# Kernel optimization log

Measured on AMD Instinct MI355X. Metric: run time of the kernel, lower is better.

## Reference

```python
import jax, jax.numpy as jnp
import numpy as np

N_NODES = 50000
N_EDGES = 800000
N_GRAPHS = 512
D = 128
NUM_GIN_LAYERS = 4
BN_EPS = 1e-5


def setup_inputs() -> dict:
    key = jax.random.key(0)
    ks = jax.random.split(key, 10)
    h = jax.random.normal(ks[0], (N_NODES, D), dtype=jnp.float32)
    src = jax.random.randint(ks[1], (N_EDGES,), 0, N_NODES, dtype=jnp.int32)
    dst = jax.random.randint(ks[2], (N_EDGES,), 0, N_NODES, dtype=jnp.int32)
    graph_id = jnp.sort(jax.random.randint(ks[3], (N_NODES,), 0, N_GRAPHS, dtype=jnp.int32))
    scale = 1.0 / np.sqrt(D)
    W1s = jax.random.normal(ks[4], (NUM_GIN_LAYERS, D, D), dtype=jnp.float32) * scale
    W2s = jax.random.normal(ks[5], (NUM_GIN_LAYERS, D, D), dtype=jnp.float32) * scale
    bn1_g = jnp.ones((NUM_GIN_LAYERS, D), jnp.float32)
    bn1_b = jnp.zeros((NUM_GIN_LAYERS, D), jnp.float32)
    bn2_g = jnp.ones((NUM_GIN_LAYERS, D), jnp.float32)
    bn2_b = jnp.zeros((NUM_GIN_LAYERS, D), jnp.float32)
    pred_W = jax.random.normal(ks[6], (NUM_GIN_LAYERS + 1, D, D), dtype=jnp.float32) * scale
    pred_b = jnp.zeros((NUM_GIN_LAYERS + 1, D), jnp.float32)
    return {"h": h, "src": src, "dst": dst, "graph_id": graph_id,
            "W1s": W1s, "W2s": W2s, "bn1_g": bn1_g, "bn1_b": bn1_b,
            "bn2_g": bn2_g, "bn2_b": bn2_b, "pred_W": pred_W, "pred_b": pred_b}


def _batch_norm(x, gamma, beta):
    # training-mode BN over the node axis
    mean = jnp.mean(x, axis=0)
    var = jnp.var(x, axis=0)
    return (x - mean) * jax.lax.rsqrt(var + BN_EPS) * gamma + beta


def reference(h, src, dst, graph_id, W1s, W2s, bn1_g, bn1_b, bn2_g, bn2_b, pred_W, pred_b):
    n = h.shape[0]
    hidden_rep = [h]
    for i in range(NUM_GIN_LAYERS):
        # GINConv, eps=0: (1+eps)*h + sum over in-neighbors (scatter-sum over edges)
        agg = jax.ops.segment_sum(h[src], dst, num_segments=n)
        z = h + agg
        # two-layer MLP: Linear(no bias) -> BN -> ReLU -> Linear(no bias)
        z = jax.nn.relu(_batch_norm(z @ W1s[i], bn1_g[i], bn1_b[i]))
        z = z @ W2s[i]
        # outer BN + ReLU
        h = jax.nn.relu(_batch_norm(z, bn2_g[i], bn2_b[i]))
        hidden_rep.append(h)
    # graph readout: per-graph max pool over each layer's representation,
    # then per-layer linear prediction summed (dropout is identity in eval)
    score = jnp.zeros((N_GRAPHS, pred_W.shape[-1]), h.dtype)
    for i, hr in enumerate(hidden_rep):
        pooled = jax.ops.segment_max(hr, graph_id, num_segments=N_GRAPHS,
                                     indices_are_sorted=True)
        score = score + pooled @ pred_W[i] + pred_b[i]
    return score
```

## Files before the change

kernel.cpp:

```cpp
#include <hip/hip_runtime.h>

#define N_NODES 50000
#define N_EDGES 800000
#define N_GRAPHS 512
#define DIM 128
#define NLAYERS 4
#define BN_EPS 1e-5f
#define NTILE (N_NODES / 16)
#define POIS ((int)0xAAAAAAAA)
#define NREP 8

#define NBUCK 80
#define CAPB 12288
#define EPB 1600
#define NBIN 500

typedef unsigned short u16;
typedef float f32x2 __attribute__((ext_vector_type(2)));
typedef float f32x4 __attribute__((ext_vector_type(4)));
typedef short bf16x8 __attribute__((ext_vector_type(8)));

__device__ __forceinline__ short f2bs(float f) {
    union { float f; unsigned u; } v; v.f = f;
    unsigned r = v.u + 0x7FFFu + ((v.u >> 16) & 1u);
    return (short)(r >> 16);
}
__device__ __forceinline__ float bu2f(unsigned u) {
    union { unsigned u; float f; } v; v.u = u << 16;
    return v.f;
}
__device__ __forceinline__ unsigned packbf(float x, float y) {
    return ((unsigned)(u16)f2bs(y) << 16) | (unsigned)(u16)f2bs(x);
}

__device__ __forceinline__ void foldbn(const float* __restrict__ st,
                                       const float* __restrict__ gamma,
                                       const float* __restrict__ beta,
                                       float* absm, int tid) {
    if (tid < 128) {
        float s = 0.f, sq = 0.f;
#pragma unroll
        for (int j = 0; j < NREP; j++) {
            s += st[j * 256 + tid];
            sq += st[j * 256 + 128 + tid];
        }
        float mean = s * (1.f / N_NODES);
        float var = sq * (1.f / N_NODES) - mean * mean;
        float a = gamma[tid] * rsqrtf(var + BN_EPS);
        absm[tid] = a;
        absm[DIM + tid] = beta[tid] - mean * a;
    }
}

__global__ __launch_bounds__(256) void k_prep(const float* __restrict__ h,
                                              const float* __restrict__ W1s,
                                              const float* __restrict__ W2s,
                                              const int* __restrict__ gid,
                                              unsigned* __restrict__ hb,
                                              short* __restrict__ wt,
                                              int* __restrict__ gs, int* __restrict__ ge) {
    int gtid = blockIdx.x * 256 + threadIdx.x;
    {
        f32x4 v = *(const f32x4*)(h + gtid * 4);
        uint2 pp;
        pp.x = packbf(v.x, v.y);
        pp.y = packbf(v.z, v.w);
        *(uint2*)(hb + gtid * 2) = pp;
    }
    if (gtid < 8 * 16384) {
        int m = gtid >> 14, r = gtid & 16383, n = r >> 7, k = r & 127;
        const float* W = (m < 4) ? (W1s + m * 16384) : (W2s + (m - 4) * 16384);
        wt[gtid] = f2bs(W[k * DIM + n]);
    }
    if (gtid < N_NODES) {
        int g = gid[gtid];
        if (gtid == 0 || gid[gtid - 1] != g) gs[g] = gtid;
        if (gtid == N_NODES - 1 || gid[gtid + 1] != g) ge[g] = gtid + 1;
    }
}

__global__ __launch_bounds__(256) void k_bin(const int* __restrict__ src,
                                             const int* __restrict__ dst,
                                             unsigned* __restrict__ eb,
                                             int* __restrict__ gcur) {
    __shared__ int hist[NBUCK], base[NBUCK], lcur[NBUCK];
    int bid = blockIdx.x, tid = threadIdx.x;
    if (tid < NBUCK) hist[tid] = 0;
    __syncthreads();
    int e0 = bid * EPB;
    unsigned rec[7]; int rb[7];
#pragma unroll
    for (int k = 0; k < 7; k++) {
        int idx = tid + k * 256;
        rb[k] = -1;
        if (idx < EPB) {
            int s = src[e0 + idx], d = dst[e0 + idx];
            rec[k] = ((unsigned)d << 16) | (unsigned)s;
            int x = d / 6250;
            int sub = (d - x * 6250) / 625;
            rb[k] = x + 8 * sub;
            atomicAdd(&hist[rb[k]], 1);
        }
    }
    __syncthreads();
    if (tid < NBUCK) {
        int old = atomicAdd(&gcur[tid], hist[tid]);
        base[tid] = old - POIS;
        lcur[tid] = 0;
    }
    __syncthreads();
#pragma unroll
    for (int k = 0; k < 7; k++) {
        if (rb[k] >= 0) {
            int p = atomicAdd(&lcur[rb[k]], 1);
            eb[rb[k] * CAPB + base[rb[k]] + p] = rec[k];
        }
    }
}

__global__ __launch_bounds__(256) void k_fill2(const unsigned* __restrict__ eb,
                                               const int* __restrict__ gcur,
                                               int* __restrict__ begA,
                                               int* __restrict__ endA,
                                               int* __restrict__ eix) {
    __shared__ int hist[625], begL[625], sm[256];
    int bid = blockIdx.x, tid = threadIdx.x;
    int x = bid & 7, sub = bid >> 3;
    int n0 = x * 6250 + sub * 625;
    int mybase = 0, mycnt = 0;
    for (int r = 0; r < NBUCK; r++) {
        int c = gcur[r] - POIS;
        int rx = r & 7, rs = r >> 3;
        if (rx < x || (rx == x && rs < sub)) mybase += c;
        if (r == bid) mycnt = c;
    }
    for (int i = tid; i < 625; i += 256) hist[i] = 0;
    __syncthreads();
    const unsigned* my = eb + bid * CAPB;
    for (int i = tid; i < mycnt; i += 256) {
        int dl = (int)(my[i] >> 16) - n0;
        atomicAdd(&hist[dl], 1);
    }
    __syncthreads();
    int carry = 0;
    for (int c = 0; c < 3; c++) {
        int idx = c * 256 + tid;
        int v = (idx < 625) ? hist[idx] : 0;
        int xv = v;
        sm[tid] = xv; __syncthreads();
#pragma unroll
        for (int d = 1; d < 256; d <<= 1) {
            int y = (tid >= d) ? sm[tid - d] : 0;
            __syncthreads();
            sm[tid] = xv = xv + y;
            __syncthreads();
        }
        if (idx < 625) begL[idx] = mybase + carry + xv - v;
        int ct = sm[255];
        __syncthreads();
        carry += ct;
    }
    __syncthreads();
    for (int i = tid; i < 625; i += 256) {
        int b = begL[i];
        begA[n0 + i] = b;
        endA[n0 + i] = b + hist[i];
    }
    __syncthreads();
    for (int i = tid; i < mycnt; i += 256) {
        unsigned rc = my[i];
        int dl = (int)(rc >> 16) - n0;
        int p = atomicAdd(&begL[dl], 1);
        eix[p] = (int)(rc & 0xFFFFu);
    }
}

__global__ __launch_bounds__(256) void k_pool0(const float* __restrict__ h,
                                               const int* __restrict__ gs,
                                               const int* __restrict__ ge,
                                               float* __restrict__ pool4) {
    __shared__ f32x2 psm[256];
    int pb = blockIdx.x, tid = threadIdx.x;
    int g = pb >> 2, sub = pb & 3;
    int c2 = (tid & 63) * 2, ro = tid >> 6;
    int beg = gs[g], end = ge[g];
    f32x2 mx = (f32x2){-3.402823e38f, -3.402823e38f};
    if (beg >= 0 && end <= N_NODES) {
        for (int r = beg + sub * 4 + ro; r < end; r += 16) {
            f32x2 v = *(const f32x2*)(h + r * DIM + c2);
            mx.x = fmaxf(mx.x, v.x);
            mx.y = fmaxf(mx.y, v.y);
        }
    }
    psm[tid] = mx;
    __syncthreads();
    if (ro == 0) {
        f32x2 m0 = psm[tid], m1 = psm[tid + 64], m2 = psm[tid + 128], m3 = psm[tid + 192];
        m0.x = fmaxf(fmaxf(m0.x, m1.x), fmaxf(m2.x, m3.x));
        m0.y = fmaxf(fmaxf(m0.y, m1.y), fmaxf(m2.y, m3.y));
        *(f32x2*)(pool4 + pb * DIM + c2) = m0;
    }
}

template <bool XF>
__global__ __launch_bounds__(256) void k_gather(const unsigned* __restrict__ hp,
                                                const int* __restrict__ begA,
                                                const int* __restrict__ endA,
                                                const int* __restrict__ eix,
                                                const float* __restrict__ absg,
                                                unsigned* __restrict__ Za) {
    int node = blockIdx.x * 4 + (threadIdx.x >> 6);
    int lane = threadIdx.x & 63;
    float a0 = 1.f, a1 = 1.f, b0 = 0.f, b1 = 0.f;
    if (XF) {
        a0 = absg[2 * lane]; a1 = absg[2 * lane + 1];
        b0 = absg[DIM + 2 * lane]; b1 = absg[DIM + 2 * lane + 1];
    }
#define TX(w, rx, ry)                                     \
    {                                                     \
        float _x = bu2f((w) & 0xffffu), _y = bu2f((w) >> 16); \
        if (XF) {                                         \
            _x = fmaxf(a0 * _x + b0, 0.f);                \
            _y = fmaxf(a1 * _y + b1, 0.f);                \
        }                                                 \
        rx += _x; ry += _y;                               \
    }
    float ax = 0.f, ay = 0.f;
    TX(hp[node * 64 + lane], ax, ay);
    int beg = begA[node];
    int end = endA[node];
    int e = beg;
    for (; e + 8 <= end; e += 8) {
        int s0 = eix[e], s1 = eix[e + 1], s2 = eix[e + 2], s3 = eix[e + 3];
        int s4 = eix[e + 4], s5 = eix[e + 5], s6 = eix[e + 6], s7 = eix[e + 7];
        unsigned w0 = hp[s0 * 64 + lane], w1 = hp[s1 * 64 + lane];
        unsigned w2 = hp[s2 * 64 + lane], w3 = hp[s3 * 64 + lane];
        unsigned w4 = hp[s4 * 64 + lane], w5 = hp[s5 * 64 + lane];
        unsigned w6 = hp[s6 * 64 + lane], w7 = hp[s7 * 64 + lane];
        TX(w0, ax, ay); TX(w1, ax, ay); TX(w2, ax, ay); TX(w3, ax, ay);
        TX(w4, ax, ay); TX(w5, ax, ay); TX(w6, ax, ay); TX(w7, ax, ay);
    }
    for (; e < end; e++) {
        unsigned ww = hp[eix[e] * 64 + lane];
        TX(ww, ax, ay);
    }
#undef TX
    Za[node * 64 + lane] = packbf(ax, ay);
}

template <bool XF>
__global__ __launch_bounds__(256, 2) void k_gemm(const unsigned* __restrict__ X,
                                                 const short* __restrict__ wt,
                                                 const float* __restrict__ statsPrev,
                                                 const float* __restrict__ gamma,
                                                 const float* __restrict__ beta,
                                                 unsigned* __restrict__ OUT,
                                                 float* __restrict__ statsDst) {
    __shared__ float tbuf[4][16][68];
    __shared__ float absm[256];
    __shared__ float smst[256];
    const int tid = threadIdx.x, bid = blockIdx.x;
    const int lane = tid & 63, wid = tid >> 6;
    const int ln15 = lane & 15, q = lane >> 4;
    float (*buf)[68] = tbuf[wid];

    bf16x8 bfr[8][4];
#pragma unroll
    for (int tl = 0; tl < 8; tl++)
#pragma unroll
        for (int s = 0; s < 4; s++)
            bfr[tl][s] = *(const bf16x8*)(wt + (tl * 16 + ln15) * DIM + s * 32 + q * 8);

    if (XF) foldbn(statsPrev, gamma, beta, absm, tid);
    smst[tid] = 0.f;
    __syncthreads();

    float sac[8], qac[8];
#pragma unroll
    for (int t = 0; t < 8; t++) { sac[t] = 0.f; qac[t] = 0.f; }

    f32x4 aA[4], aB[4], bA[4], bB[4];
    if (XF) {
#pragma unroll
        for (int s = 0; s < 4; s++) {
            int k0 = s * 32 + q * 8;
            aA[s] = *(const f32x4*)(absm + k0);
            aB[s] = *(const f32x4*)(absm + k0 + 4);
            bA[s] = *(const f32x4*)(absm + DIM + k0);
            bB[s] = *(const f32x4*)(absm + DIM + k0 + 4);
        }
    }

    for (int tile = bid * 4 + wid; tile < NTILE; tile += gridDim.x * 4) {
        const unsigned* xr = X + (tile * 16 + ln15) * 64;
        bf16x8 afr[4];
        if constexpr (!XF) {
#pragma unroll
            for (int s = 0; s < 4; s++)
                afr[s] = *(const bf16x8*)(xr + s * 16 + q * 4);
        } else {
#pragma unroll
            for (int s = 0; s < 4; s++) {
                uint4 wv = *(const uint4*)(xr + s * 16 + q * 4);
                float v0 = fmaxf(aA[s].x * bu2f(wv.x & 0xffffu) + bA[s].x, 0.f);
                float v1 = fmaxf(aA[s].y * bu2f(wv.x >> 16) + bA[s].y, 0.f);
                float v2 = fmaxf(aA[s].z * bu2f(wv.y & 0xffffu) + bA[s].z, 0.f);
                float v3 = fmaxf(aA[s].w * bu2f(wv.y >> 16) + bA[s].w, 0.f);
                float v4 = fmaxf(aB[s].x * bu2f(wv.z & 0xffffu) + bB[s].x, 0.f);
                float v5 = fmaxf(aB[s].y * bu2f(wv.z >> 16) + bB[s].y, 0.f);
                float v6 = fmaxf(aB[s].z * bu2f(wv.w & 0xffffu) + bB[s].z, 0.f);
                float v7 = fmaxf(aB[s].w * bu2f(wv.w >> 16) + bB[s].w, 0.f);
                bf16x8 a;
                a[0] = f2bs(v0); a[1] = f2bs(v1); a[2] = f2bs(v2); a[3] = f2bs(v3);
                a[4] = f2bs(v4); a[5] = f2bs(v5); a[6] = f2bs(v6); a[7] = f2bs(v7);
                afr[s] = a;
            }
        }
        f32x4 acc[8];
#pragma unroll
        for (int t = 0; t < 8; t++) acc[t] = (f32x4){0.f, 0.f, 0.f, 0.f};
#pragma unroll
        for (int s = 0; s < 4; s++) {
#pragma unroll
            for (int t = 0; t < 8; t++)
                acc[t] = __builtin_amdgcn_mfma_f32_16x16x32_bf16(afr[s], bfr[t][s], acc[t], 0, 0, 0);
        }
#pragma unroll
        for (int t = 0; t < 8; t++) {
            float s_l = 0.f, q_l = 0.f;
#pragma unroll
            for (int r = 0; r < 4; r++) {
                float v = acc[t][r];
                s_l += v;
                q_l += v * v;
            }
            s_l += __shfl_xor(s_l, 16); s_l += __shfl_xor(s_l, 32);
            q_l += __shfl_xor(q_l, 16); q_l += __shfl_xor(q_l, 32);
            sac[t] += s_l;
            qac[t] += q_l;
        }
#pragma unroll
        for (int ch = 0; ch < 2; ch++) {
#pragma unroll
            for (int t2 = 0; t2 < 4; t2++) {
                int t = ch * 4 + t2;
#pragma unroll
                for (int r = 0; r < 4; r++)
                    buf[q * 4 + r][t2 * 16 + ln15] = acc[t][r];
            }
#pragma unroll
            for (int rr = 0; rr < 4; rr++) {
                int lr = rr * 4 + q;
                f32x4 v = *(const f32x4*)&buf[lr][ln15 * 4];
                uint2 pp;
                pp.x = packbf(v.x, v.y);
                pp.y = packbf(v.z, v.w);
                *(uint2*)(OUT + (tile * 16 + lr) * 64 + ch * 32 + ln15 * 2) = pp;
            }
        }
    }
    if (lane < 16) {
#pragma unroll
        for (int t = 0; t < 8; t++) {
            atomicAdd(&smst[t * 16 + ln15], sac[t]);
            atomicAdd(&smst[128 + t * 16 + ln15], qac[t]);
        }
    }
    __syncthreads();
    atomicAdd(statsDst + (bid & (NREP - 1)) * 256 + tid, smst[tid]);
}

__global__ __launch_bounds__(256) void k_pool(const unsigned* __restrict__ Zr,
                                              const float* __restrict__ stats,
                                              const float* __restrict__ gamma,
                                              const float* __restrict__ beta,
                                              const int* __restrict__ gs,
                                              const int* __restrict__ ge,
                                              float* __restrict__ pool4,
                                              float* __restrict__ absg) {
    __shared__ float absm[256];
    __shared__ f32x2 psm[256];
    int bid = blockIdx.x, tid = threadIdx.x;
    int g = bid >> 2, sub = bid & 3;
    foldbn(stats, gamma, beta, absm, tid);
    __syncthreads();
    if (bid == 0) absg[tid] = absm[tid];
    int ci = tid & 63, ro = tid >> 6;
    int beg = gs[g], end = ge[g];
    f32x2 a = *(const f32x2*)(absm + ci * 2);
    f32x2 b = *(const f32x2*)(absm + DIM + ci * 2);
    f32x2 mx = (f32x2){-3.402823e38f, -3.402823e38f};
    if (beg >= 0 && end <= N_NODES) {
        for (int r = beg + sub * 4 + ro; r < end; r += 16) {
            unsigned w = Zr[r * 64 + ci];
            float vx = fmaxf(a.x * bu2f(w & 0xffffu) + b.x, 0.f);
            float vy = fmaxf(a.y * bu2f(w >> 16) + b.y, 0.f);
            mx.x = fmaxf(mx.x, vx);
            mx.y = fmaxf(mx.y, vy);
        }
    }
    psm[tid] = mx;
    __syncthreads();
    if (ro == 0) {
        f32x2 m0 = psm[tid], m1 = psm[tid + 64], m2 = psm[tid + 128], m3 = psm[tid + 192];
        m0.x = fmaxf(fmaxf(m0.x, m1.x), fmaxf(m2.x, m3.x));
        m0.y = fmaxf(fmaxf(m0.y, m1.y), fmaxf(m2.y, m3.y));
        *(f32x2*)(pool4 + bid * DIM + ci * 2) = m0;
    }
}

__global__ void k_readout(const float* __restrict__ pool4, const float* __restrict__ predW,
                          const float* __restrict__ predb, float* __restrict__ out) {
    __shared__ float pl[5][DIM];
    int g = blockIdx.x, c = threadIdx.x;
    for (int l = 0; l < 5; l++) {
        const float* p = pool4 + l * (N_GRAPHS * 4 * DIM) + g * 4 * DIM + c;
        float m = fmaxf(fmaxf(p[0], p[DIM]), fmaxf(p[2 * DIM], p[3 * DIM]));
        pl[l][c] = m;
    }
    __syncthreads();
    float acc = 0.f;
    for (int l = 0; l < 5; l++) {
        acc += predb[l * DIM + c];
        const float* W = predW + l * DIM * DIM;
#pragma unroll 8
        for (int k = 0; k < DIM; k++) acc += pl[l][k] * W[k * DIM + c];
    }
    out[g * DIM + c] = acc;
}

extern "C" void kernel_launch(void* const* d_in, const int* in_sizes, int n_in,
                              void* d_out, int out_size, void* d_ws, size_t ws_size,
                              hipStream_t stream) {
    const float* h_in = (const float*)d_in[0];
    const int* src = (const int*)d_in[1];
    const int* dst = (const int*)d_in[2];
    const int* gid = (const int*)d_in[3];
    const float* W1s = (const float*)d_in[4];
    const float* W2s = (const float*)d_in[5];
    const float* bn1g = (const float*)d_in[6];
    const float* bn1b = (const float*)d_in[7];
    const float* bn2g = (const float*)d_in[8];
    const float* bn2b = (const float*)d_in[9];
    const float* predW = (const float*)d_in[10];
    const float* predb = (const float*)d_in[11];

    char* ws = (char*)d_ws;
    unsigned* hb = (unsigned*)(ws);
    unsigned* Za = (unsigned*)(ws + 12800000);
    unsigned* Yb = (unsigned*)(ws + 25600000);
    unsigned* Zr = (unsigned*)(ws + 38400000);
    short* wt = (short*)(ws + 51200000);
    float* stats = (float*)(ws + 51462144);
    float* pool4 = (float*)(ws + 51527680);
    int* begA = (int*)(ws + 56770560);
    int* endA = (int*)(ws + 56970560);
    int* eix = (int*)(ws + 57372800);
    int* gs = (int*)(ws + 60572800);
    int* ge = (int*)(ws + 60574848);
    float* absg = (float*)(ws + 60576896);
    unsigned* eb = (unsigned*)(ws + 25600000);
    int* gcur = (int*)(ws + 25600000 + 8388608);
    float* out = (float*)d_out;

    const int PSTRIDE = N_GRAPHS * 4 * DIM;

    k_prep<<<6250, 256, 0, stream>>>(h_in, W1s, W2s, gid, hb, wt, gs, ge);
    k_bin<<<NBIN, 256, 0, stream>>>(src, dst, eb, gcur);
    k_fill2<<<NBUCK, 256, 0, stream>>>(eb, gcur, begA, endA, eix);
    k_pool0<<<2048, 256, 0, stream>>>(h_in, gs, ge, pool4);

    for (int l = 0; l < NLAYERS; l++) {
        if (l == 0)
            k_gather<false><<<12500, 256, 0, stream>>>(hb, begA, endA, eix, absg, Za);
        else
            k_gather<true><<<12500, 256, 0, stream>>>(Zr, begA, endA, eix, absg, Za);
        k_gemm<false><<<512, 256, 0, stream>>>(Za, wt + l * 16384, nullptr, nullptr, nullptr,
                                               Yb, stats + (l * 2) * (NREP * 256));
        k_gemm<true><<<512, 256, 0, stream>>>(Yb, wt + (4 + l) * 16384,
                                              stats + (l * 2) * (NREP * 256), bn1g + l * DIM,
                                              bn1b + l * DIM, Zr,
                                              stats + (l * 2 + 1) * (NREP * 256));
        k_pool<<<2048, 256, 0, stream>>>(Zr, stats + (l * 2 + 1) * (NREP * 256),
                                         bn2g + l * DIM, bn2b + l * DIM, gs, ge,
                                         pool4 + (l + 1) * PSTRIDE, absg);
    }
    k_readout<<<512, 128, 0, stream>>>(pool4, predW, predb, out);
}
```

Baseline: 511.2 us.

## Merge preprocessing kernels, narrow edge indices to u16, parallelize readout over layers

Combines prep with edge binning and the CSR fill with layer-0 pooling into two launches, using block-index ranges so independent work shares a grid. This removes two kernel launches and their serialization gaps. Edge source indices are stored as 16-bit values, which halves gather index traffic; this is only valid while node indices fit in 16 bits, and N_NODES is 50000, so they do. The readout now uses 640 threads so each layer's matvec runs in parallel, followed by a shared-memory reduction.

```diff
diff --git a/kernel.cpp b/kernel.cpp
--- a/kernel.cpp
+++ b/kernel.cpp
@@ -52,14 +52,55 @@
     }
 }
 
-__global__ __launch_bounds__(256) void k_prep(const float* __restrict__ h,
-                                              const float* __restrict__ W1s,
-                                              const float* __restrict__ W2s,
-                                              const int* __restrict__ gid,
-                                              unsigned* __restrict__ hb,
-                                              short* __restrict__ wt,
-                                              int* __restrict__ gs, int* __restrict__ ge) {
-    int gtid = blockIdx.x * 256 + threadIdx.x;
+__global__ __launch_bounds__(256) void k_prepbin(const float* __restrict__ h,
+                                                 const float* __restrict__ W1s,
+                                                 const float* __restrict__ W2s,
+                                                 const int* __restrict__ gid,
+                                                 const int* __restrict__ src,
+                                                 const int* __restrict__ dst,
+                                                 unsigned* __restrict__ hb,
+                                                 short* __restrict__ wt,
+                                                 int* __restrict__ gs, int* __restrict__ ge,
+                                                 unsigned* __restrict__ eb,
+                                                 int* __restrict__ gcur) {
+    __shared__ int hist[NBUCK], base[NBUCK], lcur[NBUCK];
+    int bid = blockIdx.x, tid = threadIdx.x;
+    if (bid >= 6250) {
+        int bbid = bid - 6250;
+        if (tid < NBUCK) hist[tid] = 0;
+        __syncthreads();
+        int e0 = bbid * EPB;
+        unsigned rec[7]; int rb[7];
+#pragma unroll
+        for (int k = 0; k < 7; k++) {
+            int idx = tid + k * 256;
+            rb[k] = -1;
+            if (idx < EPB) {
+                int s = src[e0 + idx], d = dst[e0 + idx];
+                rec[k] = ((unsigned)d << 16) | (unsigned)s;
+                int x = d / 6250;
+                int sub = (d - x * 6250) / 625;
+                rb[k] = x + 8 * sub;
+                atomicAdd(&hist[rb[k]], 1);
+            }
+        }
+        __syncthreads();
+        if (tid < NBUCK) {
+            int old = atomicAdd(&gcur[tid], hist[tid]);
+            base[tid] = old - POIS;
+            lcur[tid] = 0;
+        }
+        __syncthreads();
+#pragma unroll
+        for (int k = 0; k < 7; k++) {
+            if (rb[k] >= 0) {
+                int p = atomicAdd(&lcur[rb[k]], 1);
+                eb[rb[k] * CAPB + base[rb[k]] + p] = rec[k];
+            }
+        }
+        return;
+    }
+    int gtid = bid * 256 + tid;
     {
         f32x4 v = *(const f32x4*)(h + gtid * 4);
         uint2 pp;
@@ -79,108 +120,70 @@
     }
 }
 
-__global__ __launch_bounds__(256) void k_bin(const int* __restrict__ src,
-                                             const int* __restrict__ dst,
-                                             unsigned* __restrict__ eb,
-                                             int* __restrict__ gcur) {
-    __shared__ int hist[NBUCK], base[NBUCK], lcur[NBUCK];
+__global__ __launch_bounds__(256) void k_fillpool0(const unsigned* __restrict__ eb,
+                                                   const int* __restrict__ gcur,
+                                                   int* __restrict__ begA,
+                                                   int* __restrict__ endA,
+                                                   u16* __restrict__ eix,
+                                                   const float* __restrict__ h,
+                                                   const int* __restrict__ gs,
+                                                   const int* __restrict__ ge,
+                                                   float* __restrict__ pool4) {
+    __shared__ int hist[625], begL[625], sm[256];
+    __shared__ f32x2 psm[256];
     int bid = blockIdx.x, tid = threadIdx.x;
-    if (tid < NBUCK) hist[tid] = 0;
-    __syncthreads();
-    int e0 = bid * EPB;
-    unsigned rec[7]; int rb[7];
-#pragma unroll
-    for (int k = 0; k < 7; k++) {
-        int idx = tid + k * 256;
-        rb[k] = -1;
-        if (idx < EPB) {
-            int s = src[e0 + idx], d = dst[e0 + idx];
-            rec[k] = ((unsigned)d << 16) | (unsigned)s;
-            int x = d / 6250;
-            int sub = (d - x * 6250) / 625;
-            rb[k] = x + 8 * sub;
-            atomicAdd(&hist[rb[k]], 1);
-        }
-    }
-    __syncthreads();
-    if (tid < NBUCK) {
-        int old = atomicAdd(&gcur[tid], hist[tid]);
-        base[tid] = old - POIS;
-        lcur[tid] = 0;
-    }
-    __syncthreads();
-#pragma unroll
-    for (int k = 0; k < 7; k++) {
-        if (rb[k] >= 0) {
-            int p = atomicAdd(&lcur[rb[k]], 1);
-            eb[rb[k] * CAPB + base[rb[k]] + p] = rec[k];
-        }
-    }
-}
-
-__global__ __launch_bounds__(256) void k_fill2(const unsigned* __restrict__ eb,
-                                               const int* __restrict__ gcur,
-                                               int* __restrict__ begA,
-                                               int* __restrict__ endA,
-                                               int* __restrict__ eix) {
-    __shared__ int hist[625], begL[625], sm[256];
-    int bid = blockIdx.x, tid = threadIdx.x;
-    int x = bid & 7, sub = bid >> 3;
-    int n0 = x * 6250 + sub * 625;
-    int mybase = 0, mycnt = 0;
-    for (int r = 0; r < NBUCK; r++) {
-        int c = gcur[r] - POIS;
-        int rx = r & 7, rs = r >> 3;
-        if (rx < x || (rx == x && rs < sub)) mybase += c;
-        if (r == bid) mycnt = c;
-    }
-    for (int i = tid; i < 625; i += 256) hist[i] = 0;
-    __syncthreads();
-    const unsigned* my = eb + bid * CAPB;
-    for (int i = tid; i < mycnt; i += 256) {
-        int dl = (int)(my[i] >> 16) - n0;
-        atomicAdd(&hist[dl], 1);
-    }
-    __syncthreads();
-    int carry = 0;
-    for (int c = 0; c < 3; c++) {
-        int idx = c * 256 + tid;
-        int v = (idx < 625) ? hist[idx] : 0;
-        int xv = v;
-        sm[tid] = xv; __syncthreads();
-#pragma unroll
-        for (int d = 1; d < 256; d <<= 1) {
-            int y = (tid >= d) ? sm[tid - d] : 0;
+    if (bid < NBUCK) {
+        int x = bid & 7, sub = bid >> 3;
+        int n0 = x * 6250 + sub * 625;
+        int mybase = 0, mycnt = 0;
+        for (int r = 0; r < NBUCK; r++) {
+            int c = gcur[r] - POIS;
+            int rx = r & 7, rs = r >> 3;
+            if (rx < x || (rx == x && rs < sub)) mybase += c;
+            if (r == bid) mycnt = c;
+        }
+        for (int i = tid; i < 625; i += 256) hist[i] = 0;
+        __syncthreads();
+        const unsigned* my = eb + bid * CAPB;
+        for (int i = tid; i < mycnt; i += 256) {
+            int dl = (int)(my[i] >> 16) - n0;
+            atomicAdd(&hist[dl], 1);
+        }
+        __syncthreads();
+        int carry = 0;
+        for (int c = 0; c < 3; c++) {
+            int idx = c * 256 + tid;
+            int v = (idx < 625) ? hist[idx] : 0;
+            int xv = v;
+            sm[tid] = xv; __syncthreads();
+#pragma unroll
+            for (int d = 1; d < 256; d <<= 1) {
+                int y = (tid >= d) ? sm[tid - d] : 0;
+                __syncthreads();
+                sm[tid] = xv = xv + y;
+                __syncthreads();
+            }
+            if (idx < 625) begL[idx] = mybase + carry + xv - v;
+            int ct = sm[255];
             __syncthreads();
-            sm[tid] = xv = xv + y;
-            __syncthreads();
-        }
-        if (idx < 625) begL[idx] = mybase + carry + xv - v;
-        int ct = sm[255];
-        __syncthreads();
-        carry += ct;
-    }
-    __syncthreads();
-    for (int i = tid; i < 625; i += 256) {
-        int b = begL[i];
-        begA[n0 + i] = b;
-        endA[n0 + i] = b + hist[i];
-    }
-    __syncthreads();
-    for (int i = tid; i < mycnt; i += 256) {
-        unsigned rc = my[i];
-        int dl = (int)(rc >> 16) - n0;
-        int p = atomicAdd(&begL[dl], 1);
-        eix[p] = (int)(rc & 0xFFFFu);
-    }
-}
-
-__global__ __launch_bounds__(256) void k_pool0(const float* __restrict__ h,
-                                               const int* __restrict__ gs,
-                                               const int* __restrict__ ge,
-                                               float* __restrict__ pool4) {
-    __shared__ f32x2 psm[256];
-    int pb = blockIdx.x, tid = threadIdx.x;
+            carry += ct;
+        }
+        __syncthreads();
+        for (int i = tid; i < 625; i += 256) {
+            int b = begL[i];
+            begA[n0 + i] = b;
+            endA[n0 + i] = b + hist[i];
+        }
+        __syncthreads();
+        for (int i = tid; i < mycnt; i += 256) {
+            unsigned rc = my[i];
+            int dl = (int)(rc >> 16) - n0;
+            int p = atomicAdd(&begL[dl], 1);
+            eix[p] = (u16)(rc & 0xFFFFu);
+        }
+        return;
+    }
+    int pb = bid - NBUCK;
     int g = pb >> 2, sub = pb & 3;
     int c2 = (tid & 63) * 2, ro = tid >> 6;
     int beg = gs[g], end = ge[g];
@@ -206,7 +209,7 @@
 __global__ __launch_bounds__(256) void k_gather(const unsigned* __restrict__ hp,
                                                 const int* __restrict__ begA,
                                                 const int* __restrict__ endA,
-                                                const int* __restrict__ eix,
+                                                const u16* __restrict__ eix,
                                                 const float* __restrict__ absg,
                                                 unsigned* __restrict__ Za) {
     int node = blockIdx.x * 4 + (threadIdx.x >> 6);
@@ -409,24 +412,33 @@
     }
 }
 
-__global__ void k_readout(const float* __restrict__ pool4, const float* __restrict__ predW,
-                          const float* __restrict__ predb, float* __restrict__ out) {
+__global__ __launch_bounds__(640) void k_readout(const float* __restrict__ pool4,
+                                                 const float* __restrict__ predW,
+                                                 const float* __restrict__ predb,
+                                                 float* __restrict__ out) {
     __shared__ float pl[5][DIM];
-    int g = blockIdx.x, c = threadIdx.x;
-    for (int l = 0; l < 5; l++) {
+    __shared__ float ps[5][DIM];
+    int g = blockIdx.x, t = threadIdx.x;
+    int l = t >> 7, c = t & 127;
+    {
         const float* p = pool4 + l * (N_GRAPHS * 4 * DIM) + g * 4 * DIM + c;
         float m = fmaxf(fmaxf(p[0], p[DIM]), fmaxf(p[2 * DIM], p[3 * DIM]));
         pl[l][c] = m;
     }
     __syncthreads();
     float acc = 0.f;
-    for (int l = 0; l < 5; l++) {
-        acc += predb[l * DIM + c];
-        const float* W = predW + l * DIM * DIM;
+    const float* W = predW + l * DIM * DIM;
+    const float* prow = pl[l];
 #pragma unroll 8
-        for (int k = 0; k < DIM; k++) acc += pl[l][k] * W[k * DIM + c];
-    }
-    out[g * DIM + c] = acc;
+    for (int k = 0; k < DIM; k++) acc += prow[k] * W[k * DIM + c];
+    ps[l][c] = acc;
+    __syncthreads();
+    if (t < DIM) {
+        float s = 0.f;
+#pragma unroll
+        for (int ll = 0; ll < 5; ll++) s += ps[ll][c] + predb[ll * DIM + c];
+        out[g * DIM + c] = s;
+    }
 }
 
 extern "C" void kernel_launch(void* const* d_in, const int* in_sizes, int n_in,
@@ -455,7 +467,7 @@
     float* pool4 = (float*)(ws + 51527680);
     int* begA = (int*)(ws + 56770560);
     int* endA = (int*)(ws + 56970560);
-    int* eix = (int*)(ws + 57372800);
+    u16* eix = (u16*)(ws + 57372800);
     int* gs = (int*)(ws + 60572800);
     int* ge = (int*)(ws + 60574848);
     float* absg = (float*)(ws + 60576896);
@@ -465,10 +477,8 @@
 
     const int PSTRIDE = N_GRAPHS * 4 * DIM;
 
-    k_prep<<<6250, 256, 0, stream>>>(h_in, W1s, W2s, gid, hb, wt, gs, ge);
-    k_bin<<<NBIN, 256, 0, stream>>>(src, dst, eb, gcur);
-    k_fill2<<<NBUCK, 256, 0, stream>>>(eb, gcur, begA, endA, eix);
-    k_pool0<<<2048, 256, 0, stream>>>(h_in, gs, ge, pool4);
+    k_prepbin<<<6750, 256, 0, stream>>>(h_in, W1s, W2s, gid, src, dst, hb, wt, gs, ge, eb, gcur);
+    k_fillpool0<<<NBUCK + 2048, 256, 0, stream>>>(eb, gcur, begA, endA, eix, h_in, gs, ge, pool4);
 
     for (int l = 0; l < NLAYERS; l++) {
         if (l == 0)
@@ -485,5 +495,5 @@
                                          bn2g + l * DIM, bn2b + l * DIM, gs, ge,
                                          pool4 + (l + 1) * PSTRIDE, absg);
     }
-    k_readout<<<512, 128, 0, stream>>>(pool4, predW, predb, out);
-}
+    k_readout<<<512, 640, 0, stream>>>(pool4, predW, predb, out);
+}
```

Measured after the change: 488.3 us. -4.5%, faster.
